# Kernel optimization log

Measured on AMD Instinct MI355X. Metric: run time of the kernel, lower is better.

The kernel has to match this reference:

```python
import jax, jax.numpy as jnp
import numpy as np

BS, SL, D, NH = 2, 2048, 1024, 16
HD = D // NH
SCALE = D ** (-0.5)  # NOTE: source scales by full model dim, not head dim


def setup_inputs() -> dict:
    key = jax.random.key(0)
    k1, k2, k3 = jax.random.split(key, 3)
    return {
        "input_sequence": jax.random.normal(k1, (BS, SL, D), dtype=jnp.float32),
        "w_qkv": jax.random.normal(k2, (D, 3 * D), dtype=jnp.float32) * (D ** -0.5),
        "w_out": jax.random.normal(k3, (D, D), dtype=jnp.float32) * (D ** -0.5),
    }


def reference(input_sequence, w_qkv, w_out):
    bs, sl, od = input_sequence.shape
    nh, hd = NH, od // NH
    qkv = input_sequence @ w_qkv                      # [bs, sl, 3d]
    q, k, v = jnp.split(qkv, 3, axis=-1)              # each [bs, sl, d]
    q = q * SCALE

    def heads(x):  # [bs, sl, d] -> [bs, nh, sl, hd]
        return x.reshape(bs, sl, nh, hd).transpose(0, 2, 1, 3)

    q, k, v = heads(q), heads(k), heads(v)
    scores = jnp.einsum("bhqd,bhkd->bhqk", q, k)      # [bs, nh, sl, sl]
    weights = jax.nn.softmax(scores, axis=-1)
    ctx = jnp.einsum("bhqk,bhkd->bhqd", weights, v)   # [bs, nh, sl, hd]
    ctx = ctx.transpose(0, 2, 1, 3).reshape(bs, sl, od)
    return ctx @ w_out
```

## Files before the change

### kernel.cpp

```cpp
#include <hip/hip_runtime.h>
#include <cstdint>
#include <cstddef>

typedef float f32x4 __attribute__((ext_vector_type(4)));
typedef float f32x16 __attribute__((ext_vector_type(16)));
typedef __bf16 bf16x8 __attribute__((ext_vector_type(8)));
typedef __bf16 bf16x4 __attribute__((ext_vector_type(4)));
typedef uint32_t u32x4 __attribute__((ext_vector_type(4)));

static constexpr int BSZ = 2, SL = 2048, DM = 1024, NH = 16, HD = 64;
static constexpr int MROWS = BSZ * SL;
static constexpr float LOG2E = 1.4426950408889634f;
static constexpr float QSCALE = 0.03125f * LOG2E;

__device__ __forceinline__ f32x4 mfma16(bf16x8 a, bf16x8 b, f32x4 c) {
    return __builtin_amdgcn_mfma_f32_16x16x32_bf16(a, b, c, 0, 0, 0);
}
__device__ __forceinline__ f32x16 mfma32(bf16x8 a, bf16x8 b, f32x16 c) {
    return __builtin_amdgcn_mfma_f32_32x32x16_bf16(a, b, c, 0, 0, 0);
}
__device__ __forceinline__ uint32_t pkbf(float lo, float hi) {
    uint16_t a = __builtin_bit_cast(uint16_t, (__bf16)lo);
    uint16_t b = __builtin_bit_cast(uint16_t, (__bf16)hi);
    return ((uint32_t)b << 16) | (uint32_t)a;
}
__device__ __forceinline__ void gload16(const void* g, void* l) {
    __builtin_amdgcn_global_load_lds(
        (const __attribute__((address_space(1))) uint32_t*)g,
        (__attribute__((address_space(3))) uint32_t*)l, 16, 0, 0);
}

__global__ __launch_bounds__(256) void r7_cast(const float* __restrict__ in,
                                               __bf16* __restrict__ out, int n) {
    int i = (blockIdx.x * 256 + threadIdx.x) * 4;
    if (i >= n) return;
    float4 v = *(const float4*)&in[i];
    bf16x4 o;
    o.x = (__bf16)v.x; o.y = (__bf16)v.y; o.z = (__bf16)v.z; o.w = (__bf16)v.w;
    *(bf16x4*)&out[i] = o;
}

__global__ __launch_bounds__(256) void r7_transpose_cast(const float* __restrict__ in,
                                                         __bf16* __restrict__ out,
                                                         int R, int C) {
    __shared__ float tile[32][33];
    int c0 = blockIdx.x * 32, r0 = blockIdx.y * 32;
    int tx = threadIdx.x & 31, ty = threadIdx.x >> 5;
#pragma unroll
    for (int i = 0; i < 32; i += 8)
        tile[ty + i][tx] = in[(size_t)(r0 + ty + i) * C + c0 + tx];
    __syncthreads();
#pragma unroll
    for (int i = 0; i < 32; i += 8)
        out[(size_t)(c0 + ty + i) * R + r0 + tx] = (__bf16)tile[tx][ty + i];
}

template <int EPI, int BN>
__global__ __launch_bounds__(256) void r7_gemm(
    const __bf16* __restrict__ A, const __bf16* __restrict__ Bt,
    float* __restrict__ ob, int M, int N, int K,
    __bf16* __restrict__ qb, __bf16* __restrict__ kb, __bf16* __restrict__ vtb)
{
    constexpr int BM = 128, BK = 32;
    constexpr int FN = BN / 32;
    __shared__ __bf16 As[BM * BK];
    __shared__ __bf16 Bs[BN * BK];
    const int tid  = threadIdx.x;
    const int m0   = blockIdx.y * BM, n0 = blockIdx.x * BN;
    const int wave = tid >> 6, lane = tid & 63;
    const int lcol = lane & 15, lgrp = lane >> 4;
    const int wm   = (wave >> 1) * 64, wn = (wave & 1) * (BN / 2);
    const int grow = lane >> 2, gcol = (lane & 3) * 8;

    f32x4 acc[4][FN] = {};

    for (int k0 = 0; k0 < K; k0 += BK) {
        {
            const int cA0 = 2 * wave;
            gload16(&A[(size_t)(m0 + cA0 * 16 + grow) * K + k0 + gcol], &As[cA0 * 512]);
            gload16(&A[(size_t)(m0 + (cA0 + 1) * 16 + grow) * K + k0 + gcol], &As[(cA0 + 1) * 512]);
            if constexpr (BN == 128) {
                gload16(&Bt[(size_t)(n0 + cA0 * 16 + grow) * K + k0 + gcol], &Bs[cA0 * 512]);
                gload16(&Bt[(size_t)(n0 + (cA0 + 1) * 16 + grow) * K + k0 + gcol], &Bs[(cA0 + 1) * 512]);
            } else {
                gload16(&Bt[(size_t)(n0 + wave * 16 + grow) * K + k0 + gcol], &Bs[wave * 512]);
            }
        }
        __syncthreads();
        bf16x8 af[4], bfr[FN];
#pragma unroll
        for (int f = 0; f < 4; ++f)
            af[f] = *(const bf16x8*)&As[(wm + f * 16 + lcol) * BK + lgrp * 8];
#pragma unroll
        for (int f = 0; f < FN; ++f)
            bfr[f] = *(const bf16x8*)&Bs[(wn + f * 16 + lcol) * BK + lgrp * 8];
#pragma unroll
        for (int fm = 0; fm < 4; ++fm)
#pragma unroll
            for (int fn = 0; fn < FN; ++fn)
                acc[fm][fn] = mfma16(af[fm], bfr[fn], acc[fm][fn]);
        __syncthreads();
    }

#pragma unroll
    for (int fm = 0; fm < 4; ++fm) {
#pragma unroll
        for (int fn = 0; fn < FN; ++fn) {
            int n = n0 + wn + fn * 16 + lcol;
#pragma unroll
            for (int r = 0; r < 4; ++r) {
                int m = m0 + wm + fm * 16 + lgrp * 4 + r;
                float v = acc[fm][fn][r];
                if (EPI == 0) {
                    ob[(size_t)m * N + n] = v;
                } else {
                    int sec = n >> 10, nm = n & 1023;
                    int h = nm >> 6, d = nm & 63;
                    int b = m >> 11, s = m & 2047;
                    size_t bh = (size_t)(b * NH + h);
                    if (sec == 0)      qb[(bh * SL + s) * HD + d]  = (__bf16)(v * QSCALE);
                    else if (sec == 1) kb[(bh * SL + s) * HD + d]  = (__bf16)v;
                    else               vtb[(bh * HD + d) * SL + s] = (__bf16)v;
                }
            }
        }
    }
}

#define PV_STEP(a0,a1,a2,a3,a4,a5,a6,a7, KS) do {                               \
    uint32_t w0 = pkbf(a0, a1), w1 = pkbf(a2, a3);                              \
    uint32_t w2 = pkbf(a4, a5), w3 = pkbf(a6, a7);                              \
    asm volatile("v_permlane32_swap_b32 %0, %1" : "+v"(w0), "+v"(w2));          \
    asm volatile("v_permlane32_swap_b32 %0, %1" : "+v"(w1), "+v"(w3));          \
    u32x4 pw = {w0, w1, w2, w3};                                                \
    bf16x8 pf = __builtin_bit_cast(bf16x8, pw);                                 \
    const int cv = (((KS) * 2 + h) ^ swz8) * 8;                                 \
    bf16x8 vf0 = *(const bf16x8*)&Vl[lq * 64 + cv];                             \
    bf16x8 vf1 = *(const bf16x8*)&Vl[(lq + 32) * 64 + cv];                      \
    accT0 = mfma32(vf0, pf, accT0);                                             \
    accT1 = mfma32(vf1, pf, accT1);                                             \
} while (0)

__global__ __launch_bounds__(256) void r7_attn(
    const __bf16* __restrict__ qb, const __bf16* __restrict__ kb,
    const __bf16* __restrict__ vtb, __bf16* __restrict__ part0,
    __bf16* __restrict__ part1, float* __restrict__ ml)
{
    __shared__ __bf16 arena[16384];
    const int bh    = blockIdx.y;
    const int split = blockIdx.z;
    const int tid   = threadIdx.x;
    const int wave  = tid >> 6, lane = tid & 63;
    const int lq = lane & 31, h = lane >> 5;
    const int swz8 = lq & 7;
    const int q0 = blockIdx.x * 128 + wave * 32;
    const int kv0 = split * (SL / 2);

    const __bf16* Q  = qb  + ((size_t)bh * SL + q0) * HD;
    const __bf16* Kg = kb  + (size_t)bh * SL * HD;
    const __bf16* Vg = vtb + (size_t)bh * HD * SL;

    const int rA = tid >> 3, cA = tid & 7;
    const int sA = cA ^ (rA & 7);
    const int oA = rA * 64 + sA * 8;

    bf16x8 qf[4];
#pragma unroll
    for (int t = 0; t < 4; ++t)
        qf[t] = *(const bf16x8*)&Q[(size_t)lq * HD + t * 16 + h * 8];

    f32x16 accT0 = {}, accT1 = {};
    float m_run = -1e30f, l_run = 0.f;

    const __bf16* KgA = Kg + (size_t)(kv0 + rA) * HD + cA * 8;
    const __bf16* VgA = Vg + (size_t)rA * SL + kv0 + cA * 8;
    int4 kA = *(const int4*)(KgA);
    int4 kB = *(const int4*)(KgA + (size_t)32 * HD);
    int4 vA = *(const int4*)(VgA);
    int4 vB = *(const int4*)(VgA + (size_t)32 * SL);

    constexpr int NT = SL / 2 / 64;
    for (int t = 0; t < NT; ++t) {
        const int cur = t & 1;
        {
            __bf16* dK = &arena[cur * 8192 + oA];
            __bf16* dV = dK + 4096;
            *(int4*)dK = kA;  *(int4*)(dK + 2048) = kB;
            *(int4*)dV = vA;  *(int4*)(dV + 2048) = vB;
        }
        if (t + 1 < NT) {
            const __bf16* nK = KgA + (size_t)(t + 1) * 64 * HD;
            const __bf16* nV = VgA + (size_t)(t + 1) * 64;
            kA = *(const int4*)(nK);
            kB = *(const int4*)(nK + (size_t)32 * HD);
            vA = *(const int4*)(nV);
            vB = *(const int4*)(nV + (size_t)32 * SL);
        }
        __syncthreads();

        const __bf16* Kl = &arena[cur * 8192];
        const __bf16* Vl = Kl + 4096;

        f32x16 s0 = {}, s1 = {};
        __builtin_amdgcn_s_setprio(1);
#pragma unroll
        for (int t4 = 0; t4 < 4; ++t4) {
            const int cv = ((t4 * 2 + h) ^ swz8) * 8;
            bf16x8 kf0 = *(const bf16x8*)&Kl[lq * 64 + cv];
            bf16x8 kf1 = *(const bf16x8*)&Kl[(lq + 32) * 64 + cv];
            s0 = mfma32(kf0, qf[t4], s0);
            s1 = mfma32(kf1, qf[t4], s1);
        }
        __builtin_amdgcn_s_setprio(0);

        float t16[16];
#pragma unroll
        for (int i = 0; i < 16; ++i) t16[i] = fmaxf(s0[i], s1[i]);
#pragma unroll
        for (int i = 0; i < 8; ++i) t16[i] = fmaxf(t16[i], t16[i + 8]);
#pragma unroll
        for (int i = 0; i < 4; ++i) t16[i] = fmaxf(t16[i], t16[i + 4]);
        float mt = fmaxf(fmaxf(t16[0], t16[1]), fmaxf(t16[2], t16[3]));
        mt = fmaxf(mt, __shfl_xor(mt, 32));
        if (__any(mt > m_run + 8.f)) {
            float mn = fmaxf(m_run, mt);
            float alpha = exp2f(m_run - mn);
            m_run = mn;
            l_run *= alpha;
            accT0 *= alpha;
            accT1 *= alpha;
        }
        float p0[16], p1[16];
#pragma unroll
        for (int i = 0; i < 16; ++i) {
            p0[i] = exp2f(s0[i] - m_run);
            p1[i] = exp2f(s1[i] - m_run);
        }
        float a16[16];
#pragma unroll
        for (int i = 0; i < 16; ++i) a16[i] = p0[i] + p1[i];
#pragma unroll
        for (int i = 0; i < 8; ++i) a16[i] += a16[i + 8];
#pragma unroll
        for (int i = 0; i < 4; ++i) a16[i] += a16[i + 4];
        float lt = (a16[0] + a16[1]) + (a16[2] + a16[3]);
        lt += __shfl_xor(lt, 32);
        l_run += lt;

        __builtin_amdgcn_s_setprio(1);
        PV_STEP(p0[0], p0[1], p0[2], p0[3], p0[4], p0[5], p0[6], p0[7], 0);
        PV_STEP(p0[8], p0[9], p0[10], p0[11], p0[12], p0[13], p0[14], p0[15], 1);
        PV_STEP(p1[0], p1[1], p1[2], p1[3], p1[4], p1[5], p1[6], p1[7], 2);
        PV_STEP(p1[8], p1[9], p1[10], p1[11], p1[12], p1[13], p1[14], p1[15], 3);
        __builtin_amdgcn_s_setprio(0);
    }

    if (h == 0)
        ml[split * (32 * SL) + bh * SL + q0 + lq] = m_run + __log2f(l_run);

    __syncthreads();
    __bf16* Osw = &arena[wave * 2304];
    float inv = 1.f / l_run;
#pragma unroll
    for (int r = 0; r < 16; ++r) {
        int d0 = (r & 3) + 8 * (r >> 2) + 4 * h;
        Osw[lq * 72 + d0]      = (__bf16)(accT0[r] * inv);
        Osw[lq * 72 + 32 + d0] = (__bf16)(accT1[r] * inv);
    }
    asm volatile("s_waitcnt lgkmcnt(0)" ::: "memory");
    __builtin_amdgcn_sched_barrier(0);
    const int b = bh >> 4, head = bh & 15;
    const int qr = lane >> 1, seg = (lane & 1) * 32;
    __bf16* pbase = split == 0 ? part0 : part1;
    __bf16* dst = &pbase[((size_t)b * SL + q0 + qr) * DM + head * HD + seg];
#pragma unroll
    for (int c = 0; c < 4; ++c)
        *(bf16x8*)&dst[c * 8] = *(const bf16x8*)&Osw[qr * 72 + seg + c * 8];
}

__global__ __launch_bounds__(256) void r7_merge(
    const __bf16* __restrict__ p0, const __bf16* __restrict__ p1,
    const float* __restrict__ ml, __bf16* __restrict__ out)
{
    int idx = blockIdx.x * 256 + threadIdx.x;
    int m = idx >> 7, g = idx & 127;
    int d0 = g * 8, h = d0 >> 6;
    int b = m >> 11, q = m & 2047;
    int bhq = (b * NH + h) * SL + q;
    float ml0 = ml[bhq], ml1 = ml[32 * SL + bhq];
    float M = fmaxf(ml0, ml1);
    float w0 = exp2f(ml0 - M), w1 = exp2f(ml1 - M);
    float inv = 1.f / (w0 + w1);
    w0 *= inv; w1 *= inv;
    size_t off = (size_t)m * DM + d0;
    bf16x8 a = *(const bf16x8*)&p0[off];
    bf16x8 c = *(const bf16x8*)&p1[off];
    bf16x8 o;
#pragma unroll
    for (int j = 0; j < 8; ++j) o[j] = (__bf16)(w0 * (float)a[j] + w1 * (float)c[j]);
    *(bf16x8*)&out[off] = o;
}

extern "C" void kernel_launch(void* const* d_in, const int* in_sizes, int n_in,
                              void* d_out, int out_size, void* d_ws, size_t ws_size,
                              hipStream_t stream) {
    const float* x    = (const float*)d_in[0];
    const float* wqkv = (const float*)d_in[1];
    const float* wout = (const float*)d_in[2];
    float* out = (float*)d_out;

    __bf16* ws    = (__bf16*)d_ws;
    __bf16* xb    = ws;
    __bf16* wqkvT = xb    + (size_t)MROWS * DM;
    __bf16* woutT = wqkvT + (size_t)3 * DM * DM;
    __bf16* qbuf  = woutT + (size_t)DM * DM;
    __bf16* kbuf  = qbuf  + (size_t)MROWS * DM;
    __bf16* vtbuf = kbuf  + (size_t)MROWS * DM;
    __bf16* ctxb  = vtbuf + (size_t)MROWS * DM;
    __bf16* part0 = xb;
    __bf16* part1 = ctxb;
    float*  mlbuf = (float*)wqkvT;

    r7_cast<<<dim3((MROWS * DM) / 1024), dim3(256), 0, stream>>>(x, xb, MROWS * DM);
    r7_transpose_cast<<<dim3(96, 32), dim3(256), 0, stream>>>(wqkv, wqkvT, DM, 3 * DM);
    r7_transpose_cast<<<dim3(32, 32), dim3(256), 0, stream>>>(wout, woutT, DM, DM);

    r7_gemm<1, 128><<<dim3(24, 32), dim3(256), 0, stream>>>(
        xb, wqkvT, (float*)nullptr, MROWS, 3 * DM, DM, qbuf, kbuf, vtbuf);

    r7_attn<<<dim3(16, 32, 2), dim3(256), 0, stream>>>(
        qbuf, kbuf, vtbuf, part0, part1, mlbuf);

    r7_merge<<<dim3(2048), dim3(256), 0, stream>>>(part0, part1, mlbuf, ctxb);

    r7_gemm<0, 64><<<dim3(16, 32), dim3(256), 0, stream>>>(
        ctxb, woutT, out, MROWS, DM, DM,
        (__bf16*)nullptr, (__bf16*)nullptr, (__bf16*)nullptr);
}
```

Baseline: 160.3 us.

## Remove split-KV attention and merge kernel; use hardware exp2

Attention now processes the full KV length per block instead of splitting it in two, writing the normalized context directly and removing the merge kernel plus the partial/logsumexp buffers. Softmax exponentials use the raw hardware exp2 instruction instead of exp2f. This removes one launch and the extra partial-result memory traffic, at the cost of halving the grid size for the attention kernel, which may reduce latency hiding.

```diff
diff --git a/kernel.cpp b/kernel.cpp
--- a/kernel.cpp
+++ b/kernel.cpp
@@ -24,14 +24,21 @@
     uint16_t b = __builtin_bit_cast(uint16_t, (__bf16)hi);
     return ((uint32_t)b << 16) | (uint32_t)a;
 }
+__device__ __forceinline__ float fexp2(float x) {
+#if __has_builtin(__builtin_amdgcn_exp2f)
+    return __builtin_amdgcn_exp2f(x);
+#else
+    float r; asm volatile("v_exp_f32 %0, %1" : "=v"(r) : "v"(x)); return r;
+#endif
+}
 __device__ __forceinline__ void gload16(const void* g, void* l) {
     __builtin_amdgcn_global_load_lds(
         (const __attribute__((address_space(1))) uint32_t*)g,
         (__attribute__((address_space(3))) uint32_t*)l, 16, 0, 0);
 }
 
-__global__ __launch_bounds__(256) void r7_cast(const float* __restrict__ in,
-                                               __bf16* __restrict__ out, int n) {
+__global__ __launch_bounds__(256) void r10_cast(const float* __restrict__ in,
+                                                __bf16* __restrict__ out, int n) {
     int i = (blockIdx.x * 256 + threadIdx.x) * 4;
     if (i >= n) return;
     float4 v = *(const float4*)&in[i];
@@ -40,9 +47,9 @@
     *(bf16x4*)&out[i] = o;
 }
 
-__global__ __launch_bounds__(256) void r7_transpose_cast(const float* __restrict__ in,
-                                                         __bf16* __restrict__ out,
-                                                         int R, int C) {
+__global__ __launch_bounds__(256) void r10_transpose_cast(const float* __restrict__ in,
+                                                          __bf16* __restrict__ out,
+                                                          int R, int C) {
     __shared__ float tile[32][33];
     int c0 = blockIdx.x * 32, r0 = blockIdx.y * 32;
     int tx = threadIdx.x & 31, ty = threadIdx.x >> 5;
@@ -56,7 +63,7 @@
 }
 
 template <int EPI, int BN>
-__global__ __launch_bounds__(256) void r7_gemm(
+__global__ __launch_bounds__(256) void r10_gemm(
     const __bf16* __restrict__ A, const __bf16* __restrict__ Bt,
     float* __restrict__ ob, int M, int N, int K,
     __bf16* __restrict__ qb, __bf16* __restrict__ kb, __bf16* __restrict__ vtb)
@@ -141,20 +148,17 @@
     accT1 = mfma32(vf1, pf, accT1);                                             \
 } while (0)
 
-__global__ __launch_bounds__(256) void r7_attn(
+__global__ __launch_bounds__(256) void r10_attn(
     const __bf16* __restrict__ qb, const __bf16* __restrict__ kb,
-    const __bf16* __restrict__ vtb, __bf16* __restrict__ part0,
-    __bf16* __restrict__ part1, float* __restrict__ ml)
+    const __bf16* __restrict__ vtb, __bf16* __restrict__ ctx)
 {
     __shared__ __bf16 arena[16384];
-    const int bh    = blockIdx.y;
-    const int split = blockIdx.z;
-    const int tid   = threadIdx.x;
-    const int wave  = tid >> 6, lane = tid & 63;
+    const int bh   = blockIdx.y;
+    const int tid  = threadIdx.x;
+    const int wave = tid >> 6, lane = tid & 63;
     const int lq = lane & 31, h = lane >> 5;
     const int swz8 = lq & 7;
     const int q0 = blockIdx.x * 128 + wave * 32;
-    const int kv0 = split * (SL / 2);
 
     const __bf16* Q  = qb  + ((size_t)bh * SL + q0) * HD;
     const __bf16* Kg = kb  + (size_t)bh * SL * HD;
@@ -172,14 +176,14 @@
     f32x16 accT0 = {}, accT1 = {};
     float m_run = -1e30f, l_run = 0.f;
 
-    const __bf16* KgA = Kg + (size_t)(kv0 + rA) * HD + cA * 8;
-    const __bf16* VgA = Vg + (size_t)rA * SL + kv0 + cA * 8;
+    const __bf16* KgA = Kg + (size_t)rA * HD + cA * 8;
+    const __bf16* VgA = Vg + (size_t)rA * SL + cA * 8;
     int4 kA = *(const int4*)(KgA);
     int4 kB = *(const int4*)(KgA + (size_t)32 * HD);
     int4 vA = *(const int4*)(VgA);
     int4 vB = *(const int4*)(VgA + (size_t)32 * SL);
 
-    constexpr int NT = SL / 2 / 64;
+    constexpr int NT = SL / 64;
     for (int t = 0; t < NT; ++t) {
         const int cur = t & 1;
         {
@@ -224,7 +228,7 @@
         mt = fmaxf(mt, __shfl_xor(mt, 32));
         if (__any(mt > m_run + 8.f)) {
             float mn = fmaxf(m_run, mt);
-            float alpha = exp2f(m_run - mn);
+            float alpha = fexp2(m_run - mn);
             m_run = mn;
             l_run *= alpha;
             accT0 *= alpha;
@@ -233,8 +237,8 @@
         float p0[16], p1[16];
 #pragma unroll
         for (int i = 0; i < 16; ++i) {
-            p0[i] = exp2f(s0[i] - m_run);
-            p1[i] = exp2f(s1[i] - m_run);
+            p0[i] = fexp2(s0[i] - m_run);
+            p1[i] = fexp2(s1[i] - m_run);
         }
         float a16[16];
 #pragma unroll
@@ -255,12 +259,9 @@
         __builtin_amdgcn_s_setprio(0);
     }
 
-    if (h == 0)
-        ml[split * (32 * SL) + bh * SL + q0 + lq] = m_run + __log2f(l_run);
-
+    float inv = 1.f / l_run;
     __syncthreads();
     __bf16* Osw = &arena[wave * 2304];
-    float inv = 1.f / l_run;
 #pragma unroll
     for (int r = 0; r < 16; ++r) {
         int d0 = (r & 3) + 8 * (r >> 2) + 4 * h;
@@ -271,34 +272,10 @@
     __builtin_amdgcn_sched_barrier(0);
     const int b = bh >> 4, head = bh & 15;
     const int qr = lane >> 1, seg = (lane & 1) * 32;
-    __bf16* pbase = split == 0 ? part0 : part1;
-    __bf16* dst = &pbase[((size_t)b * SL + q0 + qr) * DM + head * HD + seg];
+    __bf16* dst = &ctx[((size_t)b * SL + q0 + qr) * DM + head * HD + seg];
 #pragma unroll
     for (int c = 0; c < 4; ++c)
         *(bf16x8*)&dst[c * 8] = *(const bf16x8*)&Osw[qr * 72 + seg + c * 8];
-}
-
-__global__ __launch_bounds__(256) void r7_merge(
-    const __bf16* __restrict__ p0, const __bf16* __restrict__ p1,
-    const float* __restrict__ ml, __bf16* __restrict__ out)
-{
-    int idx = blockIdx.x * 256 + threadIdx.x;
-    int m = idx >> 7, g = idx & 127;
-    int d0 = g * 8, h = d0 >> 6;
-    int b = m >> 11, q = m & 2047;
-    int bhq = (b * NH + h) * SL + q;
-    float ml0 = ml[bhq], ml1 = ml[32 * SL + bhq];
-    float M = fmaxf(ml0, ml1);
-    float w0 = exp2f(ml0 - M), w1 = exp2f(ml1 - M);
-    float inv = 1.f / (w0 + w1);
-    w0 *= inv; w1 *= inv;
-    size_t off = (size_t)m * DM + d0;
-    bf16x8 a = *(const bf16x8*)&p0[off];
-    bf16x8 c = *(const bf16x8*)&p1[off];
-    bf16x8 o;
-#pragma unroll
-    for (int j = 0; j < 8; ++j) o[j] = (__bf16)(w0 * (float)a[j] + w1 * (float)c[j]);
-    *(bf16x8*)&out[off] = o;
 }
 
 extern "C" void kernel_launch(void* const* d_in, const int* in_sizes, int n_in,
@@ -317,23 +294,17 @@
     __bf16* kbuf  = qbuf  + (size_t)MROWS * DM;
     __bf16* vtbuf = kbuf  + (size_t)MROWS * DM;
     __bf16* ctxb  = vtbuf + (size_t)MROWS * DM;
-    __bf16* part0 = xb;
-    __bf16* part1 = ctxb;
-    float*  mlbuf = (float*)wqkvT;
-
-    r7_cast<<<dim3((MROWS * DM) / 1024), dim3(256), 0, stream>>>(x, xb, MROWS * DM);
-    r7_transpose_cast<<<dim3(96, 32), dim3(256), 0, stream>>>(wqkv, wqkvT, DM, 3 * DM);
-    r7_transpose_cast<<<dim3(32, 32), dim3(256), 0, stream>>>(wout, woutT, DM, DM);
-
-    r7_gemm<1, 128><<<dim3(24, 32), dim3(256), 0, stream>>>(
+
+    r10_cast<<<dim3((MROWS * DM) / 1024), dim3(256), 0, stream>>>(x, xb, MROWS * DM);
+    r10_transpose_cast<<<dim3(96, 32), dim3(256), 0, stream>>>(wqkv, wqkvT, DM, 3 * DM);
+    r10_transpose_cast<<<dim3(32, 32), dim3(256), 0, stream>>>(wout, woutT, DM, DM);
+
+    r10_gemm<1, 128><<<dim3(24, 32), dim3(256), 0, stream>>>(
         xb, wqkvT, (float*)nullptr, MROWS, 3 * DM, DM, qbuf, kbuf, vtbuf);
 
-    r7_attn<<<dim3(16, 32, 2), dim3(256), 0, stream>>>(
-        qbuf, kbuf, vtbuf, part0, part1, mlbuf);
-
-    r7_merge<<<dim3(2048), dim3(256), 0, stream>>>(part0, part1, mlbuf, ctxb);
-
-    r7_gemm<0, 64><<<dim3(16, 32), dim3(256), 0, stream>>>(
+    r10_attn<<<dim3(16, 32), dim3(256), 0, stream>>>(qbuf, kbuf, vtbuf, ctxb);
+
+    r10_gemm<0, 64><<<dim3(16, 32), dim3(256), 0, stream>>>(
         ctxb, woutT, out, MROWS, DM, DM,
         (__bf16*)nullptr, (__bf16*)nullptr, (__bf16*)nullptr);
 }
```

Measured after the change: 141.2 us. -12.0%, faster.
